# Kernel optimization log

Hardware: AMD Instinct MI355X
Metric: run time of the kernel (lower is better)

Reference implementation:

```python
import jax, jax.numpy as jnp
import numpy as np

N = 50000       # num nodes
E = 400000      # num edges (before self loops)
IN, HID, H, OUT = 128, 64, 4, 64
SLOPE = 0.2     # PyG GATv2Conv default negative_slope


def setup_inputs() -> dict:
    key = jax.random.key(0)
    ks = jax.random.split(key, 14)
    def lin(k, fan_in, fan_out):
        return jax.random.normal(k, (fan_in, fan_out), jnp.float32) / np.sqrt(fan_in)
    return {
        "x": jax.random.normal(ks[0], (N, IN), jnp.float32),
        "edge_index": jax.random.randint(ks[1], (2, E), 0, N, jnp.int32),
        # layer 1: in=IN -> HID per head, H heads, concat
        "Wl1": lin(ks[2], IN, H * HID), "bl1": jnp.zeros((H * HID,), jnp.float32),
        "Wr1": lin(ks[3], IN, H * HID), "br1": jnp.zeros((H * HID,), jnp.float32),
        "att1": jax.random.normal(ks[4], (H, HID), jnp.float32) / np.sqrt(HID),
        "bias1": jnp.zeros((H * HID,), jnp.float32),
        # layer 2: in=H*HID -> OUT, 1 head, concat=False
        "Wl2": lin(ks[5], H * HID, OUT), "bl2": jnp.zeros((OUT,), jnp.float32),
        "Wr2": lin(ks[6], H * HID, OUT), "br2": jnp.zeros((OUT,), jnp.float32),
        "att2": jax.random.normal(ks[7], (1, OUT), jnp.float32) / np.sqrt(OUT),
        "bias2": jnp.zeros((OUT,), jnp.float32),
    }


def gatv2_conv(x, src, dst, Wl, bl, Wr, br, att, heads, out_ch, num_nodes):
    """PyG GATv2Conv (share_weights=False). src->dst aggregation at dst."""
    xl = (x @ Wl + bl).reshape(-1, heads, out_ch)  # source transform (x_j)
    xr = (x @ Wr + br).reshape(-1, heads, out_ch)  # target transform (x_i)
    m = xl[src] + xr[dst]                          # [E, H, C]
    e = jnp.sum(jax.nn.leaky_relu(m, SLOPE) * att, axis=-1)  # [E, H]
    # segment softmax over incoming edges of each dst node
    emax = jax.ops.segment_max(e, dst, num_segments=num_nodes)
    ex = jnp.exp(e - emax[dst])
    denom = jax.ops.segment_sum(ex, dst, num_segments=num_nodes)
    alpha = ex / denom[dst]                        # [E, H]
    out = jax.ops.segment_sum(alpha[:, :, None] * xl[src], dst, num_segments=num_nodes)
    return out  # [N, H, C]


def reference(x, edge_index, Wl1, bl1, Wr1, br1, att1, bias1,
              Wl2, bl2, Wr2, br2, att2, bias2):
    n = x.shape[0]
    loops = jnp.arange(n, dtype=edge_index.dtype)
    src = jnp.concatenate([edge_index[0], loops])  # add_self_loops=True
    dst = jnp.concatenate([edge_index[1], loops])
    h = gatv2_conv(x, src, dst, Wl1, bl1, Wr1, br1, att1, H, HID, n)
    h = h.reshape(n, H * HID) + bias1              # concat=True
    h = jax.nn.elu(h)                              # dropout=0.0
    o = gatv2_conv(h, src, dst, Wl2, bl2, Wr2, br2, att2, 1, OUT, n)
    return o.reshape(n, OUT) + bias2               # concat=False, heads=1
```

## Files before the change

### kernel.cpp

```cpp
#include <hip/hip_runtime.h>
#include <hip/hip_bf16.h>

typedef unsigned short u16;
typedef __attribute__((ext_vector_type(8))) short short8;
typedef __attribute__((ext_vector_type(4))) float floatx4;
typedef __attribute__((ext_vector_type(2))) float f32x2;

#define N_NODES 50000
#define N_EDGES 400000
#define ET      450000
#define F_IN    128
#define C1      256
#define HID     64
#define OUTC    64
#define SLOPE   0.2f
#define LIN1_BLOCKS 782
#define LOG2E   1.44269504089f

#if __has_builtin(__builtin_amdgcn_exp2f)
#define EXP2(x) __builtin_amdgcn_exp2f(x)
#else
#define EXP2(x) __expf((x) * 0.69314718056f)
#endif

__device__ __forceinline__ float bf2f(u16 v) {
    return __uint_as_float(((unsigned)v) << 16);
}
__device__ __forceinline__ float bflo(unsigned u) { return __uint_as_float(u << 16); }
__device__ __forceinline__ float bfhi(unsigned u) { return __uint_as_float(u & 0xffff0000u); }
__device__ __forceinline__ u16 f2bf(float f) {
    unsigned u = __float_as_uint(f);
    return (u16)((u + 0x7fffu + ((u >> 16) & 1u)) >> 16);
}
__device__ __forceinline__ f32x2 up2(unsigned u) {
    f32x2 r; r.x = bflo(u); r.y = bfhi(u); return r;
}
template<int CTRL>
__device__ __forceinline__ float dpp_add(float x) {
    return x + __int_as_float(__builtin_amdgcn_update_dpp(
        0, __float_as_int(x), CTRL, 0xF, 0xF, true));
}
__device__ __forceinline__ float red16(float p) {
    p = dpp_add<0xB1>(p);
    p = dpp_add<0x4E>(p);
    p = dpp_add<0x141>(p);
    p = dpp_add<0x140>(p);
    return p;
}
template<int CTRL>
__device__ __forceinline__ f32x2 dpp_add2(f32x2 x) {
    f32x2 o;
    o.x = __int_as_float(__builtin_amdgcn_update_dpp(
        0, __float_as_int(x.x), CTRL, 0xF, 0xF, true));
    o.y = __int_as_float(__builtin_amdgcn_update_dpp(
        0, __float_as_int(x.y), CTRL, 0xF, 0xF, true));
    return x + o;
}
__device__ __forceinline__ f32x2 red16x2(f32x2 p) {
    p = dpp_add2<0xB1>(p);
    p = dpp_add2<0x4E>(p);
    p = dpp_add2<0x141>(p);
    p = dpp_add2<0x140>(p);
    return p;
}
__device__ __forceinline__ bool detect_f32(const unsigned* __restrict__ xw) {
    unsigned w = xw[threadIdx.x & 63];
    unsigned aexp = (w >> 7) & 0xFFu;
    unsigned long long b = __ballot(aexp >= 170u || aexp <= 40u);
    return __popcll(b) >= 16;
}

__global__ __launch_bounds__(256) void convert_all_kernel(
    const unsigned* __restrict__ xw,
    const void* wl1, const void* wr1, const void* wl2, const void* wr2,
    const void* s0, const void* s1, const void* s2, const void* s3,
    const void* s4, const void* s5, const void* s6, const void* s7,
    u16* __restrict__ wt, u16* __restrict__ prm, int* __restrict__ hist)
{
    if (blockIdx.x >= 385) {
        int idx = (blockIdx.x - 385) * 256 + threadIdx.x;
        if (idx < N_NODES) hist[idx] = 0;
        return;
    }
    bool f32m = detect_f32(xw);
    if (blockIdx.x == 384) {
        for (int t = threadIdx.x; t < 1280; t += 256) {
            const void* src; int local;
            if      (t < 256)  { src = s0; local = t; }
            else if (t < 512)  { src = s1; local = t - 256; }
            else if (t < 768)  { src = s2; local = t - 512; }
            else if (t < 1024) { src = s3; local = t - 768; }
            else if (t < 1088) { src = s4; local = t - 1024; }
            else if (t < 1152) { src = s5; local = t - 1088; }
            else if (t < 1216) { src = s6; local = t - 1152; }
            else               { src = s7; local = t - 1216; }
            prm[t] = f32m ? f2bf(((const float*)src)[local]) : ((const u16*)src)[local];
        }
        return;
    }
    int t = blockIdx.x * 256 + threadIdx.x;
    const void* src; int local, k, n, dst;
    if (t < 32768) {
        src = wl1; local = t; k = local >> 8; n = local & 255;
        int ch = n >> 6, cf = (n >> 4) & 3, l16 = n & 15;
        int kk = k >> 5, quad = (k >> 3) & 3, j = k & 7;
        dst = 0 + ((ch * 4 + cf) * 4 + kk) * 512 + (quad * 16 + l16) * 8 + j;
    } else if (t < 65536) {
        src = wr1; local = t - 32768; k = local >> 8; n = local & 255;
        int ch = n >> 6, cf = (n >> 4) & 3, l16 = n & 15;
        int kk = k >> 5, quad = (k >> 3) & 3, j = k & 7;
        dst = 32768 + ((ch * 4 + cf) * 4 + kk) * 512 + (quad * 16 + l16) * 8 + j;
    } else if (t < 81920) {
        src = wl2; local = t - 65536; k = local >> 6; n = local & 63;
        int cf = n >> 4, l16 = n & 15;
        int kk = k >> 5, quad = (k >> 3) & 3, j = k & 7;
        dst = 65536 + (cf * 8 + kk) * 512 + (quad * 16 + l16) * 8 + j;
    } else {
        src = wr2; local = t - 81920; k = local >> 6; n = local & 63;
        int cf = n >> 4, l16 = n & 15;
        int kk = k >> 5, quad = (k >> 3) & 3, j = k & 7;
        dst = 81920 + (cf * 8 + kk) * 512 + (quad * 16 + l16) * 8 + j;
    }
    u16 v = f32m ? f2bf(((const float*)src)[local]) : ((const u16*)src)[local];
    wt[dst] = v;
}

__global__ __launch_bounds__(256) void scan1_kernel(const int* __restrict__ hist,
                                                    int* __restrict__ rowptr,
                                                    int* __restrict__ bsum)
{
    int t = threadIdx.x;
    int i = blockIdx.x * 256 + t;
    int v = (i < N_NODES) ? hist[i] : 0;
    __shared__ int sd[256];
    sd[t] = v;
    __syncthreads();
    #pragma unroll
    for (int ofs = 1; ofs < 256; ofs <<= 1) {
        int u = (t >= ofs) ? sd[t - ofs] : 0;
        __syncthreads();
        sd[t] += u;
        __syncthreads();
    }
    if (i < N_NODES) rowptr[i] = sd[t] - v;
    if (t == 255) bsum[blockIdx.x] = sd[255];
}

__global__ __launch_bounds__(256) void scan3_kernel(int* __restrict__ rowptr,
                                                    const int* __restrict__ bsum,
                                                    int* __restrict__ off)
{
    int t = threadIdx.x;
    int v = (t < (int)blockIdx.x) ? bsum[t] : 0;
    __shared__ int sd[256];
    sd[t] = v;
    __syncthreads();
    #pragma unroll
    for (int ofs = 1; ofs < 256; ofs <<= 1) {
        int u = (t >= ofs) ? sd[t - ofs] : 0;
        __syncthreads();
        sd[t] += u;
        __syncthreads();
    }
    int boff = sd[255];
    int i = blockIdx.x * 256 + t;
    if (i < N_NODES) {
        int r = rowptr[i] + boff;
        rowptr[i] = r;
        off[i] = r;
    }
}

__global__ __launch_bounds__(256) void scatter_kernel(const int* __restrict__ ei,
                                                      int* __restrict__ off,
                                                      int* __restrict__ src_csr)
{
    int t = blockIdx.x * 256 + threadIdx.x;
    if (t >= ET) return;
    int s, d;
    if (t < N_EDGES) { s = ei[t]; d = ei[N_EDGES + t]; } else { s = d = t - N_EDGES; }
    int pos = atomicAdd(&off[d], 1);
    src_csr[pos] = s;
}

__global__ __launch_bounds__(256) void lin1_hist_kernel(
    const u16* __restrict__ X, const u16* __restrict__ Wp,
    const u16* __restrict__ bl, const u16* __restrict__ br,
    u16* __restrict__ Yl, u16* __restrict__ Yr, int nrows,
    const int* __restrict__ ei, int* __restrict__ hist)
{
    constexpr int K = 128, N = 256, LS = K + 8;
    __shared__ __align__(16) u16 sX[64 * LS];

    if (blockIdx.x >= LIN1_BLOCKS) {
        int t = (blockIdx.x - LIN1_BLOCKS) * 256 + threadIdx.x;
        if (t < ET) {
            int d = (t < N_EDGES) ? ei[N_EDGES + t] : t - N_EDGES;
            atomicAdd(&hist[d], 1);
        }
        return;
    }

    const bool f32m = detect_f32((const unsigned*)X);
    const float* X32 = (const float*)X;
    const int row0 = blockIdx.x * 64;
    const int wave = threadIdx.x >> 6, lane = threadIdx.x & 63;
    const int quad = lane >> 4, l16 = lane & 15;

    for (int i = threadIdx.x * 8; i < 64 * K; i += 2048) {
        int r = i >> 7, c = i & 127;
        int gr = row0 + r;
        u16* dst = &sX[r * LS + c];
        if (f32m) {
            float4 v0 = make_float4(0.f, 0.f, 0.f, 0.f), v1 = v0;
            if (gr < nrows) {
                v0 = *(const float4*)&X32[(size_t)gr * K + c];
                v1 = *(const float4*)&X32[(size_t)gr * K + c + 4];
            }
            ushort4 p0, p1;
            p0.x = f2bf(v0.x); p0.y = f2bf(v0.y); p0.z = f2bf(v0.z); p0.w = f2bf(v0.w);
            p1.x = f2bf(v1.x); p1.y = f2bf(v1.y); p1.z = f2bf(v1.z); p1.w = f2bf(v1.w);
            *(ushort4*)dst = p0;
            *(ushort4*)(dst + 4) = p1;
        } else {
            uint4 v = {0u, 0u, 0u, 0u};
            if (gr < nrows) v = *(const uint4*)&X[(size_t)gr * K + c];
            *(uint4*)dst = v;
        }
    }
    __syncthreads();

    short8 a[4];
    #pragma unroll
    for (int kk = 0; kk < 4; ++kk)
        a[kk] = *(const short8*)&sX[(wave * 16 + l16) * LS + kk * 32 + quad * 8];

    const u16* wlane = Wp + lane * 8;
    for (int side = 0; side < 2; ++side) {
        const u16* bias  = side ? br : bl;
        u16* Y = side ? Yr : Yl;
        const u16* wside = wlane + side * 32768;
        for (int ch = 0; ch < 4; ++ch) {
            const u16* wch = wside + ch * 8192;
            short8 b[16];
            #pragma unroll
            for (int cf = 0; cf < 4; ++cf)
                #pragma unroll
                for (int kk = 0; kk < 4; ++kk)
                    b[cf * 4 + kk] = *(const short8*)&wch[(cf * 4 + kk) * 512];
            floatx4 acc0 = {0.f, 0.f, 0.f, 0.f}, acc1 = acc0, acc2 = acc0, acc3 = acc0;
            #pragma unroll
            for (int kk = 0; kk < 4; ++kk) {
                acc0 = __builtin_amdgcn_mfma_f32_16x16x32_bf16(a[kk], b[kk],      acc0, 0, 0, 0);
                acc1 = __builtin_amdgcn_mfma_f32_16x16x32_bf16(a[kk], b[4 + kk],  acc1, 0, 0, 0);
                acc2 = __builtin_amdgcn_mfma_f32_16x16x32_bf16(a[kk], b[8 + kk],  acc2, 0, 0, 0);
                acc3 = __builtin_amdgcn_mfma_f32_16x16x32_bf16(a[kk], b[12 + kk], acc3, 0, 0, 0);
            }
            const int rbase = row0 + wave * 16 + quad * 4;
            #pragma unroll
            for (int cf = 0; cf < 4; ++cf) {
                const floatx4 av = (cf == 0) ? acc0 : (cf == 1) ? acc1 : (cf == 2) ? acc2 : acc3;
                const int col = ch * 64 + cf * 16 + l16;
                const float bv = bf2f(bias[col]);
                #pragma unroll
                for (int r = 0; r < 4; ++r) {
                    int row = rbase + r;
                    if (row < nrows) Y[(size_t)row * N + col] = f2bf(av[r] + bv);
                }
            }
        }
    }
}

__global__ __launch_bounds__(256) void lin2_fused_kernel(
    const u16* __restrict__ X, const u16* __restrict__ Wp,
    const u16* __restrict__ bl, const u16* __restrict__ br,
    u16* __restrict__ Yl, u16* __restrict__ Yr, int nrows)
{
    constexpr int K = 256, N = 64, LS = K + 8;
    __shared__ __align__(16) u16 sX[64 * LS];
    const int row0 = blockIdx.x * 64;
    const int wave = threadIdx.x >> 6, lane = threadIdx.x & 63;
    const int quad = lane >> 4, l16 = lane & 15;

    for (int i = threadIdx.x * 8; i < 64 * K; i += 2048) {
        int r = i >> 8, c = i & 255;
        int gr = row0 + r;
        uint4 v = {0u, 0u, 0u, 0u};
        if (gr < nrows) v = *(const uint4*)&X[(size_t)gr * K + c];
        *(uint4*)&sX[r * LS + c] = v;
    }
    __syncthreads();

    short8 a[8];
    #pragma unroll
    for (int kk = 0; kk < 8; ++kk)
        a[kk] = *(const short8*)&sX[(wave * 16 + l16) * LS + kk * 32 + quad * 8];

    const u16* wlane = Wp + lane * 8;
    for (int side = 0; side < 2; ++side) {
        const u16* bias  = side ? br : bl;
        u16* Y = side ? Yr : Yl;
        const u16* wside = wlane + side * 16384;
        #pragma unroll
        for (int cf = 0; cf < 4; ++cf) {
            short8 b[8];
            #pragma unroll
            for (int kk = 0; kk < 8; ++kk)
                b[kk] = *(const short8*)&wside[(cf * 8 + kk) * 512];
            floatx4 acc = {0.f, 0.f, 0.f, 0.f};
            #pragma unroll
            for (int kk = 0; kk < 8; ++kk)
                acc = __builtin_amdgcn_mfma_f32_16x16x32_bf16(a[kk], b[kk], acc, 0, 0, 0);
            const int rbase = row0 + wave * 16 + quad * 4;
            const int col = cf * 16 + l16;
            const float bv = bf2f(bias[col]);
            #pragma unroll
            for (int r = 0; r < 4; ++r) {
                int row = rbase + r;
                if (row < nrows) Y[(size_t)row * N + col] = f2bf(acc[r] + bv);
            }
        }
    }
}

__global__ __launch_bounds__(64, 6) void node1_kernel(
    const u16* __restrict__ xl, const u16* __restrict__ xr,
    const int* __restrict__ rowptr, const int* __restrict__ hist,
    const int* __restrict__ src_csr, const u16* __restrict__ att,
    const u16* __restrict__ bias, u16* __restrict__ hout)
{
    const int d = blockIdx.x;
    const int l = threadIdx.x;
    const int start = __builtin_amdgcn_readfirstlane(rowptr[d]);
    const int deg = __builtin_amdgcn_readfirstlane(hist[d]);
    const int dm1 = deg - 1;
    const u16* __restrict__ xlp = xl + l * 4;

    uint2 auv = *(const uint2*)&att[l * 4];
    const f32x2 atA = up2(auv.x) * LOG2E, atB = up2(auv.y) * LOG2E;
    uint2 ruv = *(const uint2*)&xr[(size_t)d * C1 + l * 4];
    const f32x2 rA = up2(ruv.x), rB = up2(ruv.y);

    float m = -1e30f, la = 0.f;
    f32x2 accA = {0.f, 0.f}, accB = {0.f, 0.f};

    int s0 = __builtin_amdgcn_readfirstlane(src_csr[start]);
    int s1 = __builtin_amdgcn_readfirstlane(src_csr[start + min(1, dm1)]);
    int s2 = __builtin_amdgcn_readfirstlane(src_csr[start + min(2, dm1)]);
    int s3 = __builtin_amdgcn_readfirstlane(src_csr[start + min(3, dm1)]);
    uint2 u0 = *(const uint2*)&xlp[(size_t)s0 * C1];
    uint2 u1 = *(const uint2*)&xlp[(size_t)s1 * C1];
    uint2 u2 = *(const uint2*)&xlp[(size_t)s2 * C1];
    uint2 u3 = *(const uint2*)&xlp[(size_t)s3 * C1];
    int t0 = __builtin_amdgcn_readfirstlane(src_csr[start + min(4, dm1)]);
    int t1 = __builtin_amdgcn_readfirstlane(src_csr[start + min(5, dm1)]);
    int t2 = __builtin_amdgcn_readfirstlane(src_csr[start + min(6, dm1)]);
    int t3 = __builtin_amdgcn_readfirstlane(src_csr[start + min(7, dm1)]);
    uint2 v0 = *(const uint2*)&xlp[(size_t)t0 * C1];
    uint2 v1q = *(const uint2*)&xlp[(size_t)t1 * C1];
    uint2 v2q = *(const uint2*)&xlp[(size_t)t2 * C1];
    uint2 v3q = *(const uint2*)&xlp[(size_t)t3 * C1];

    int j = 0;
    for (; j + 4 <= deg; j += 4) {
        const uint2 c0 = u0, c1 = u1, c2 = u2, c3 = u3;
        u0 = v0; u1 = v1q; u2 = v2q; u3 = v3q;
        const int jn = j + 8;
        if (jn < deg) {
            int q0 = __builtin_amdgcn_readfirstlane(src_csr[start + jn]);
            int q1 = __builtin_amdgcn_readfirstlane(src_csr[start + min(jn + 1, dm1)]);
            int q2 = __builtin_amdgcn_readfirstlane(src_csr[start + min(jn + 2, dm1)]);
            int q3 = __builtin_amdgcn_readfirstlane(src_csr[start + min(jn + 3, dm1)]);
            v0  = *(const uint2*)&xlp[(size_t)q0 * C1];
            v1q = *(const uint2*)&xlp[(size_t)q1 * C1];
            v2q = *(const uint2*)&xlp[(size_t)q2 * C1];
            v3q = *(const uint2*)&xlp[(size_t)q3 * C1];
        }
        f32x2 x0A = up2(c0.x), x0B = up2(c0.y);
        f32x2 x1A = up2(c1.x), x1B = up2(c1.y);
        f32x2 x2A = up2(c2.x), x2B = up2(c2.y);
        f32x2 x3A = up2(c3.x), x3B = up2(c3.y);
        f32x2 t, pv;
        t = x0A + rA; t = __builtin_elementwise_max(t, t * SLOPE); pv  = t * atA;
        t = x0B + rB; t = __builtin_elementwise_max(t, t * SLOPE); pv += t * atB;
        float p0 = pv.x + pv.y;
        t = x1A + rA; t = __builtin_elementwise_max(t, t * SLOPE); pv  = t * atA;
        t = x1B + rB; t = __builtin_elementwise_max(t, t * SLOPE); pv += t * atB;
        float p1 = pv.x + pv.y;
        t = x2A + rA; t = __builtin_elementwise_max(t, t * SLOPE); pv  = t * atA;
        t = x2B + rB; t = __builtin_elementwise_max(t, t * SLOPE); pv += t * atB;
        float p2 = pv.x + pv.y;
        t = x3A + rA; t = __builtin_elementwise_max(t, t * SLOPE); pv  = t * atA;
        t = x3B + rB; t = __builtin_elementwise_max(t, t * SLOPE); pv += t * atB;
        float p3 = pv.x + pv.y;
        f32x2 P01 = {p0, p1}, P23 = {p2, p3};
        P01 = red16x2(P01);
        P23 = red16x2(P23);
        p0 = P01.x; p1 = P01.y; p2 = P23.x; p3 = P23.y;
        float pm = fmaxf(fmaxf(p0, p1), fmaxf(p2, p3));
        if (__any(pm > m)) {
            float mn = fmaxf(m, pm);
            float sc = EXP2(m - mn);
            la *= sc; accA *= sc; accB *= sc;
            m = mn;
        }
        float w0 = EXP2(p0 - m);
        float w1 = EXP2(p1 - m);
        float w2 = EXP2(p2 - m);
        float w3 = EXP2(p3 - m);
        la += w0 + w1 + w2 + w3;
        accA += x0A * w0 + x1A * w1 + x2A * w2 + x3A * w3;
        accB += x0B * w0 + x1B * w1 + x2B * w2 + x3B * w3;
    }
    if (j < deg) {
        const bool v1 = j + 1 < deg, v2 = j + 2 < deg;
        f32x2 x0A = up2(u0.x), x0B = up2(u0.y);
        f32x2 x1A = up2(u1.x), x1B = up2(u1.y);
        f32x2 x2A = up2(u2.x), x2B = up2(u2.y);
        f32x2 t, pv;
        t = x0A + rA; t = __builtin_elementwise_max(t, t * SLOPE); pv  = t * atA;
        t = x0B + rB; t = __builtin_elementwise_max(t, t * SLOPE); pv += t * atB;
        float p0 = pv.x + pv.y;
        t = x1A + rA; t = __builtin_elementwise_max(t, t * SLOPE); pv  = t * atA;
        t = x1B + rB; t = __builtin_elementwise_max(t, t * SLOPE); pv += t * atB;
        float p1 = pv.x + pv.y;
        t = x2A + rA; t = __builtin_elementwise_max(t, t * SLOPE); pv  = t * atA;
        t = x2B + rB; t = __builtin_elementwise_max(t, t * SLOPE); pv += t * atB;
        float p2 = pv.x + pv.y;
        f32x2 P01 = {p0, p1};
        P01 = red16x2(P01);
        p0 = P01.x; p1 = P01.y;
        p2 = red16(p2);
        float pm = p0;
        if (v1) pm = fmaxf(pm, p1);
        if (v2) pm = fmaxf(pm, p2);
        if (__any(pm > m)) {
            float mn = fmaxf(m, pm);
            float sc = EXP2(m - mn);
            la *= sc; accA *= sc; accB *= sc;
            m = mn;
        }
        float w0 = EXP2(p0 - m);
        float w1 = v1 ? EXP2(p1 - m) : 0.f;
        float w2 = v2 ? EXP2(p2 - m) : 0.f;
        la += w0 + w1 + w2;
        accA += x0A * w0 + x1A * w1 + x2A * w2;
        accB += x0B * w0 + x1B * w1 + x2B * w2;
    }
    const float inv = 1.f / la;
    const int c = l * 4;
    float o0 = accA.x * inv + bf2f(bias[c + 0]);
    float o1 = accA.y * inv + bf2f(bias[c + 1]);
    float o2 = accB.x * inv + bf2f(bias[c + 2]);
    float o3 = accB.y * inv + bf2f(bias[c + 3]);
    o0 = o0 > 0.f ? o0 : __expf(fminf(o0, 0.f)) - 1.f;
    o1 = o1 > 0.f ? o1 : __expf(fminf(o1, 0.f)) - 1.f;
    o2 = o2 > 0.f ? o2 : __expf(fminf(o2, 0.f)) - 1.f;
    o3 = o3 > 0.f ? o3 : __expf(fminf(o3, 0.f)) - 1.f;
    ushort4 o;
    o.x = f2bf(o0); o.y = f2bf(o1); o.z = f2bf(o2); o.w = f2bf(o3);
    *(ushort4*)&hout[(size_t)d * C1 + c] = o;
}

__global__ __launch_bounds__(64, 8) void node2_kernel(
    const u16* __restrict__ xl, const u16* __restrict__ xr,
    const int* __restrict__ rowptr, const int* __restrict__ hist,
    const int* __restrict__ src_csr, const u16* __restrict__ att,
    const u16* __restrict__ bias, void* __restrict__ outp,
    const unsigned* __restrict__ xorig)
{
    const bool f32o = detect_f32(xorig);
    const int d = blockIdx.x;
    const int l = threadIdx.x;
    const int start = __builtin_amdgcn_readfirstlane(rowptr[d]);
    const int deg = __builtin_amdgcn_readfirstlane(hist[d]);
    const int dm1 = deg - 1;
    const int g = l >> 4, sub = l & 15;
    const int c0 = sub * 4;
    const u16* __restrict__ xlp = xl + c0;

    uint2 auv = *(const uint2*)&att[c0];
    const f32x2 atA = up2(auv.x) * LOG2E, atB = up2(auv.y) * LOG2E;
    uint2 ruv = *(const uint2*)&xr[(size_t)d * OUTC + c0];
    const f32x2 rA = up2(ruv.x), rB = up2(ruv.y);

    float m = -1e30f, la = 0.f;
    f32x2 accA = {0.f, 0.f}, accB = {0.f, 0.f};

    int sA0 = src_csr[start + min(g, dm1)];
    int sA1 = src_csr[start + min(g + 4, dm1)];
    uint2 uA0 = *(const uint2*)&xlp[(size_t)sA0 * OUTC];
    uint2 uA1 = *(const uint2*)&xlp[(size_t)sA1 * OUTC];
    int sB0 = src_csr[start + min(g + 8, dm1)];
    int sB1 = src_csr[start + min(g + 12, dm1)];
    uint2 uB0 = *(const uint2*)&xlp[(size_t)sB0 * OUTC];
    uint2 uB1 = *(const uint2*)&xlp[(size_t)sB1 * OUTC];

    for (int j = 0; j < deg; j += 8) {
        const bool val0 = j + g < deg, val1 = j + g + 4 < deg;
        const uint2 e0 = uA0, e1 = uA1;
        uA0 = uB0; uA1 = uB1;
        if (j + 8 < deg) {
            int t0 = src_csr[start + min(j + 16 + g, dm1)];
            int t1 = src_csr[start + min(j + 20 + g, dm1)];
            uB0 = *(const uint2*)&xlp[(size_t)t0 * OUTC];
            uB1 = *(const uint2*)&xlp[(size_t)t1 * OUTC];
        }
        f32x2 x0A = up2(e0.x), x0B = up2(e0.y);
        f32x2 x1A = up2(e1.x), x1B = up2(e1.y);
        f32x2 t, pv;
        t = x0A + rA; t = __builtin_elementwise_max(t, t * SLOPE); pv  = t * atA;
        t = x0B + rB; t = __builtin_elementwise_max(t, t * SLOPE); pv += t * atB;
        float p0 = pv.x + pv.y;
        t = x1A + rA; t = __builtin_elementwise_max(t, t * SLOPE); pv  = t * atA;
        t = x1B + rB; t = __builtin_elementwise_max(t, t * SLOPE); pv += t * atB;
        float p1 = pv.x + pv.y;
        f32x2 P = {p0, p1};
        P = red16x2(P);
        p0 = P.x; p1 = P.y;
        float q0 = val0 ? p0 : -1e30f;
        float q1 = val1 ? p1 : -1e30f;
        float pm = fmaxf(q0, q1);
        if (__any(pm > m)) {
            float mn = fmaxf(m, pm);
            float sc = EXP2(m - mn);
            la *= sc; accA *= sc; accB *= sc;
            m = mn;
        }
        float w0 = val0 ? EXP2(p0 - m) : 0.f;
        float w1 = val1 ? EXP2(p1 - m) : 0.f;
        la += w0 + w1;
        accA += x0A * w0 + x1A * w1;
        accB += x0B * w0 + x1B * w1;
    }
    #pragma unroll
    for (int ofs = 16; ofs <= 32; ofs <<= 1) {
        float mo = __shfl_xor(m, ofs);
        float lo = __shfl_xor(la, ofs);
        float bax = __shfl_xor(accA.x, ofs);
        float bay = __shfl_xor(accA.y, ofs);
        float bbx = __shfl_xor(accB.x, ofs);
        float bby = __shfl_xor(accB.y, ofs);
        float mn = fmaxf(m, mo);
        float e0 = EXP2(m - mn), e1 = EXP2(mo - mn);
        la = la * e0 + lo * e1;
        accA.x = accA.x * e0 + bax * e1;
        accA.y = accA.y * e0 + bay * e1;
        accB.x = accB.x * e0 + bbx * e1;
        accB.y = accB.y * e0 + bby * e1;
        m = mn;
    }
    if (g == 0) {
        const float inv = 1.f / la;
        float v0 = accA.x * inv + bf2f(bias[c0 + 0]);
        float v1 = accA.y * inv + bf2f(bias[c0 + 1]);
        float v2 = accB.x * inv + bf2f(bias[c0 + 2]);
        float v3 = accB.y * inv + bf2f(bias[c0 + 3]);
        if (f32o) {
            float4 o = make_float4(v0, v1, v2, v3);
            *(float4*)&((float*)outp)[(size_t)d * OUTC + c0] = o;
        } else {
            ushort4 o;
            o.x = f2bf(v0); o.y = f2bf(v1); o.z = f2bf(v2); o.w = f2bf(v3);
            *(ushort4*)&((u16*)outp)[(size_t)d * OUTC + c0] = o;
        }
    }
}

extern "C" void kernel_launch(void* const* d_in, const int* in_sizes, int n_in,
                              void* d_out, int out_size, void* d_ws, size_t ws_size,
                              hipStream_t stream)
{
    const void* x  = d_in[0];
    const int*  ei = (const int*)d_in[1];

    char* ws = (char*)d_ws;
    u16* xl1     = (u16*)(ws + 0);
    u16* xr1     = (u16*)(ws + 25600000);
    u16* hbuf    = (u16*)(ws + 51200000);
    u16* xl2     = (u16*)(ws + 0);
    u16* xr2     = (u16*)(ws + 6400000);
    int* hist    = (int*)(ws + 76800000);
    int* rowptr  = (int*)(ws + 77000000);
    int* off     = (int*)(ws + 77200000);
    int* src_csr = (int*)(ws + 77400000);
    u16* prm     = (u16*)(ws + 79200064);
    u16* wt      = (u16*)(ws + 79210240);
    int* bsum    = (int*)(ws + 79410000);

    u16* bl1   = prm + 0;
    u16* br1   = prm + 256;
    u16* att1  = prm + 512;
    u16* bias1 = prm + 768;
    u16* bl2   = prm + 1024;
    u16* br2   = prm + 1088;
    u16* att2  = prm + 1152;
    u16* bias2 = prm + 1216;
    u16* wt1   = wt + 0;
    u16* wt2   = wt + 65536;

    convert_all_kernel<<<581, 256, 0, stream>>>(
        (const unsigned*)x,
        d_in[2], d_in[4], d_in[8], d_in[10],
        d_in[3], d_in[5], d_in[6], d_in[7], d_in[9], d_in[11], d_in[12], d_in[13],
        wt, prm, hist);

    const int eb = (ET + 255) / 256;
    lin1_hist_kernel<<<LIN1_BLOCKS + eb, 256, 0, stream>>>(
        (const u16*)x, wt1, bl1, br1, xl1, xr1, N_NODES, ei, hist);

    scan1_kernel<<<196, 256, 0, stream>>>(hist, rowptr, bsum);
    scan3_kernel<<<196, 256, 0, stream>>>(rowptr, bsum, off);
    scatter_kernel<<<eb, 256, 0, stream>>>(ei, off, src_csr);

    node1_kernel<<<N_NODES, 64, 0, stream>>>(xl1, xr1, rowptr, hist, src_csr, att1, bias1, hbuf);
    lin2_fused_kernel<<<(N_NODES + 63) / 64, 256, 0, stream>>>(hbuf, wt2, bl2, br2, xl2, xr2, N_NODES);
    node2_kernel<<<N_NODES, 64, 0, stream>>>(xl2, xr2, rowptr, hist, src_csr, att2, bias2, d_out,
                                             (const unsigned*)x);
}
```

Measured before the change: 241.5 us.

## Split linear GEMMs into single-wave blocks per 16-row tile and side

Both linear kernels are restructured from 256-thread blocks that stage 64 rows in LDS into one-wave blocks. Each wave handles 16 rows and one of the two weight sides, loading its A fragments directly from global memory. This removes the LDS staging, the __syncthreads, and the row bounds checks, and gives far more independent blocks for better occupancy and latency hiding. The trade-off is that each X row is now read twice, once per side, with no LDS reuse, and there are many more tiny blocks. The histogram part also moves to 64-thread blocks.

After: 239.8 us. About the same (-0.7%).

```diff
diff --git a/kernel.cpp b/kernel.cpp
--- a/kernel.cpp
+++ b/kernel.cpp
@@ -14,7 +14,7 @@
 #define HID     64
 #define OUTC    64
 #define SLOPE   0.2f
-#define LIN1_BLOCKS 782
+#define LIN1_WAVES 6250
 #define LOG2E   1.44269504089f
 
 #if __has_builtin(__builtin_amdgcn_exp2f)
@@ -183,17 +183,14 @@
     src_csr[pos] = s;
 }
 
-__global__ __launch_bounds__(256) void lin1_hist_kernel(
+__global__ __launch_bounds__(64, 4) void lin1_hist_kernel(
     const u16* __restrict__ X, const u16* __restrict__ Wp,
     const u16* __restrict__ bl, const u16* __restrict__ br,
-    u16* __restrict__ Yl, u16* __restrict__ Yr, int nrows,
+    u16* __restrict__ Yl, u16* __restrict__ Yr,
     const int* __restrict__ ei, int* __restrict__ hist)
 {
-    constexpr int K = 128, N = 256, LS = K + 8;
-    __shared__ __align__(16) u16 sX[64 * LS];
-
-    if (blockIdx.x >= LIN1_BLOCKS) {
-        int t = (blockIdx.x - LIN1_BLOCKS) * 256 + threadIdx.x;
+    if (blockIdx.x >= LIN1_WAVES) {
+        int t = (blockIdx.x - LIN1_WAVES) * 64 + threadIdx.x;
         if (t < ET) {
             int d = (t < N_EDGES) ? ei[N_EDGES + t] : t - N_EDGES;
             atomicAdd(&hist[d], 1);
@@ -201,126 +198,100 @@
         return;
     }
 
+    const int lane = threadIdx.x;
+    const int quad = lane >> 4, l16 = lane & 15;
+    const int side = blockIdx.x & 1;
+    const int row0 = (blockIdx.x >> 1) * 16;
     const bool f32m = detect_f32((const unsigned*)X);
-    const float* X32 = (const float*)X;
-    const int row0 = blockIdx.x * 64;
-    const int wave = threadIdx.x >> 6, lane = threadIdx.x & 63;
-    const int quad = lane >> 4, l16 = lane & 15;
-
-    for (int i = threadIdx.x * 8; i < 64 * K; i += 2048) {
-        int r = i >> 7, c = i & 127;
-        int gr = row0 + r;
-        u16* dst = &sX[r * LS + c];
-        if (f32m) {
-            float4 v0 = make_float4(0.f, 0.f, 0.f, 0.f), v1 = v0;
-            if (gr < nrows) {
-                v0 = *(const float4*)&X32[(size_t)gr * K + c];
-                v1 = *(const float4*)&X32[(size_t)gr * K + c + 4];
-            }
-            ushort4 p0, p1;
-            p0.x = f2bf(v0.x); p0.y = f2bf(v0.y); p0.z = f2bf(v0.z); p0.w = f2bf(v0.w);
-            p1.x = f2bf(v1.x); p1.y = f2bf(v1.y); p1.z = f2bf(v1.z); p1.w = f2bf(v1.w);
-            *(ushort4*)dst = p0;
-            *(ushort4*)(dst + 4) = p1;
-        } else {
-            uint4 v = {0u, 0u, 0u, 0u};
-            if (gr < nrows) v = *(const uint4*)&X[(size_t)gr * K + c];
-            *(uint4*)dst = v;
-        }
-    }
-    __syncthreads();
 
     short8 a[4];
-    #pragma unroll
-    for (int kk = 0; kk < 4; ++kk)
-        a[kk] = *(const short8*)&sX[(wave * 16 + l16) * LS + kk * 32 + quad * 8];
-
-    const u16* wlane = Wp + lane * 8;
-    for (int side = 0; side < 2; ++side) {
-        const u16* bias  = side ? br : bl;
-        u16* Y = side ? Yr : Yl;
-        const u16* wside = wlane + side * 32768;
-        for (int ch = 0; ch < 4; ++ch) {
-            const u16* wch = wside + ch * 8192;
-            short8 b[16];
+    if (f32m) {
+        const float* xrow = (const float*)X + (size_t)(row0 + l16) * F_IN;
+        #pragma unroll
+        for (int kk = 0; kk < 4; ++kk) {
+            float4 v0 = *(const float4*)&xrow[kk * 32 + quad * 8];
+            float4 v1 = *(const float4*)&xrow[kk * 32 + quad * 8 + 4];
+            union { ushort4 h[2]; short8 s8; } u;
+            u.h[0].x = f2bf(v0.x); u.h[0].y = f2bf(v0.y);
+            u.h[0].z = f2bf(v0.z); u.h[0].w = f2bf(v0.w);
+            u.h[1].x = f2bf(v1.x); u.h[1].y = f2bf(v1.y);
+            u.h[1].z = f2bf(v1.z); u.h[1].w = f2bf(v1.w);
+            a[kk] = u.s8;
+        }
+    } else {
+        const u16* xrow = X + (size_t)(row0 + l16) * F_IN;
+        #pragma unroll
+        for (int kk = 0; kk < 4; ++kk)
+            a[kk] = *(const short8*)&xrow[kk * 32 + quad * 8];
+    }
+
+    const u16* wlane = Wp + side * 32768 + lane * 8;
+    const u16* bias  = side ? br : bl;
+    u16* Y = side ? Yr : Yl;
+
+    for (int ch = 0; ch < 4; ++ch) {
+        const u16* wch = wlane + ch * 8192;
+        short8 b[16];
+        #pragma unroll
+        for (int f = 0; f < 16; ++f)
+            b[f] = *(const short8*)&wch[f * 512];
+        floatx4 acc0 = {0.f, 0.f, 0.f, 0.f}, acc1 = acc0, acc2 = acc0, acc3 = acc0;
+        #pragma unroll
+        for (int kk = 0; kk < 4; ++kk) {
+            acc0 = __builtin_amdgcn_mfma_f32_16x16x32_bf16(a[kk], b[kk],      acc0, 0, 0, 0);
+            acc1 = __builtin_amdgcn_mfma_f32_16x16x32_bf16(a[kk], b[4 + kk],  acc1, 0, 0, 0);
+            acc2 = __builtin_amdgcn_mfma_f32_16x16x32_bf16(a[kk], b[8 + kk],  acc2, 0, 0, 0);
+            acc3 = __builtin_amdgcn_mfma_f32_16x16x32_bf16(a[kk], b[12 + kk], acc3, 0, 0, 0);
+        }
+        const int rbase = row0 + quad * 4;
+        #pragma unroll
+        for (int cf = 0; cf < 4; ++cf) {
+            const floatx4 av = (cf == 0) ? acc0 : (cf == 1) ? acc1 : (cf == 2) ? acc2 : acc3;
+            const int col = ch * 64 + cf * 16 + l16;
+            const float bv = bf2f(bias[col]);
             #pragma unroll
-            for (int cf = 0; cf < 4; ++cf)
-                #pragma unroll
-                for (int kk = 0; kk < 4; ++kk)
-                    b[cf * 4 + kk] = *(const short8*)&wch[(cf * 4 + kk) * 512];
-            floatx4 acc0 = {0.f, 0.f, 0.f, 0.f}, acc1 = acc0, acc2 = acc0, acc3 = acc0;
-            #pragma unroll
-            for (int kk = 0; kk < 4; ++kk) {
-                acc0 = __builtin_amdgcn_mfma_f32_16x16x32_bf16(a[kk], b[kk],      acc0, 0, 0, 0);
-                acc1 = __builtin_amdgcn_mfma_f32_16x16x32_bf16(a[kk], b[4 + kk],  acc1, 0, 0, 0);
-                acc2 = __builtin_amdgcn_mfma_f32_16x16x32_bf16(a[kk], b[8 + kk],  acc2, 0, 0, 0);
-                acc3 = __builtin_amdgcn_mfma_f32_16x16x32_bf16(a[kk], b[12 + kk], acc3, 0, 0, 0);
-            }
-            const int rbase = row0 + wave * 16 + quad * 4;
-            #pragma unroll
-            for (int cf = 0; cf < 4; ++cf) {
-                const floatx4 av = (cf == 0) ? acc0 : (cf == 1) ? acc1 : (cf == 2) ? acc2 : acc3;
-                const int col = ch * 64 + cf * 16 + l16;
-                const float bv = bf2f(bias[col]);
-                #pragma unroll
-                for (int r = 0; r < 4; ++r) {
-                    int row = rbase + r;
-                    if (row < nrows) Y[(size_t)row * N + col] = f2bf(av[r] + bv);
-                }
-            }
-        }
-    }
-}
-
-__global__ __launch_bounds__(256) void lin2_fused_kernel(
+            for (int r = 0; r < 4; ++r)
+                Y[(size_t)(rbase + r) * C1 + col] = f2bf(av[r] + bv);
+        }
+    }
+}
+
+__global__ __launch_bounds__(64, 4) void lin2_fused_kernel(
     const u16* __restrict__ X, const u16* __restrict__ Wp,
     const u16* __restrict__ bl, const u16* __restrict__ br,
-    u16* __restrict__ Yl, u16* __restrict__ Yr, int nrows)
-{
-    constexpr int K = 256, N = 64, LS = K + 8;
-    __shared__ __align__(16) u16 sX[64 * LS];
-    const int row0 = blockIdx.x * 64;
-    const int wave = threadIdx.x >> 6, lane = threadIdx.x & 63;
+    u16* __restrict__ Yl, u16* __restrict__ Yr)
+{
+    const int lane = threadIdx.x;
     const int quad = lane >> 4, l16 = lane & 15;
-
-    for (int i = threadIdx.x * 8; i < 64 * K; i += 2048) {
-        int r = i >> 8, c = i & 255;
-        int gr = row0 + r;
-        uint4 v = {0u, 0u, 0u, 0u};
-        if (gr < nrows) v = *(const uint4*)&X[(size_t)gr * K + c];
-        *(uint4*)&sX[r * LS + c] = v;
-    }
-    __syncthreads();
-
+    const int side = blockIdx.x & 1;
+    const int row0 = (blockIdx.x >> 1) * 16;
+
+    const u16* xrow = X + (size_t)(row0 + l16) * C1;
     short8 a[8];
     #pragma unroll
     for (int kk = 0; kk < 8; ++kk)
-        a[kk] = *(const short8*)&sX[(wave * 16 + l16) * LS + kk * 32 + quad * 8];
-
-    const u16* wlane = Wp + lane * 8;
-    for (int side = 0; side < 2; ++side) {
-        const u16* bias  = side ? br : bl;
-        u16* Y = side ? Yr : Yl;
-        const u16* wside = wlane + side * 16384;
-        #pragma unroll
-        for (int cf = 0; cf < 4; ++cf) {
-            short8 b[8];
-            #pragma unroll
-            for (int kk = 0; kk < 8; ++kk)
-                b[kk] = *(const short8*)&wside[(cf * 8 + kk) * 512];
-            floatx4 acc = {0.f, 0.f, 0.f, 0.f};
-            #pragma unroll
-            for (int kk = 0; kk < 8; ++kk)
-                acc = __builtin_amdgcn_mfma_f32_16x16x32_bf16(a[kk], b[kk], acc, 0, 0, 0);
-            const int rbase = row0 + wave * 16 + quad * 4;
-            const int col = cf * 16 + l16;
-            const float bv = bf2f(bias[col]);
-            #pragma unroll
-            for (int r = 0; r < 4; ++r) {
-                int row = rbase + r;
-                if (row < nrows) Y[(size_t)row * N + col] = f2bf(acc[r] + bv);
-            }
-        }
+        a[kk] = *(const short8*)&xrow[kk * 32 + quad * 8];
+
+    const u16* wlane = Wp + side * 16384 + lane * 8;
+    const u16* bias  = side ? br : bl;
+    u16* Y = side ? Yr : Yl;
+
+    #pragma unroll
+    for (int cf = 0; cf < 4; ++cf) {
+        short8 b[8];
+        #pragma unroll
+        for (int kk = 0; kk < 8; ++kk)
+            b[kk] = *(const short8*)&wlane[(cf * 8 + kk) * 512];
+        floatx4 acc = {0.f, 0.f, 0.f, 0.f};
+        #pragma unroll
+        for (int kk = 0; kk < 8; ++kk)
+            acc = __builtin_amdgcn_mfma_f32_16x16x32_bf16(a[kk], b[kk], acc, 0, 0, 0);
+        const int rbase = row0 + quad * 4;
+        const int col = cf * 16 + l16;
+        const float bv = bf2f(bias[col]);
+        #pragma unroll
+        for (int r = 0; r < 4; ++r)
+            Y[(size_t)(rbase + r) * OUTC + col] = f2bf(acc[r] + bv);
     }
 }
 
@@ -606,16 +577,16 @@
         d_in[3], d_in[5], d_in[6], d_in[7], d_in[9], d_in[11], d_in[12], d_in[13],
         wt, prm, hist);
 
-    const int eb = (ET + 255) / 256;
-    lin1_hist_kernel<<<LIN1_BLOCKS + eb, 256, 0, stream>>>(
-        (const u16*)x, wt1, bl1, br1, xl1, xr1, N_NODES, ei, hist);
+    const int eb = (ET + 63) / 64;
+    lin1_hist_kernel<<<LIN1_WAVES + eb, 64, 0, stream>>>(
+        (const u16*)x, wt1, bl1, br1, xl1, xr1, ei, hist);
 
     scan1_kernel<<<196, 256, 0, stream>>>(hist, rowptr, bsum);
     scan3_kernel<<<196, 256, 0, stream>>>(rowptr, bsum, off);
-    scatter_kernel<<<eb, 256, 0, stream>>>(ei, off, src_csr);
+    scatter_kernel<<<(ET + 255) / 256, 256, 0, stream>>>(ei, off, src_csr);
 
     node1_kernel<<<N_NODES, 64, 0, stream>>>(xl1, xr1, rowptr, hist, src_csr, att1, bias1, hbuf);
-    lin2_fused_kernel<<<(N_NODES + 63) / 64, 256, 0, stream>>>(hbuf, wt2, bl2, br2, xl2, xr2, N_NODES);
+    lin2_fused_kernel<<<LIN1_WAVES, 64, 0, stream>>>(hbuf, wt2, bl2, br2, xl2, xr2);
     node2_kernel<<<N_NODES, 64, 0, stream>>>(xl2, xr2, rowptr, hist, src_csr, att2, bias2, d_out,
                                              (const unsigned*)x);
 }
```
